# Kernel tuning notes

Measured on AMD Instinct MI355X. Metric: run time of the kernel, lower is better.

## Reference

```python
import jax, jax.numpy as jnp
import numpy as np


def setup_inputs() -> dict:
    key = jax.random.key(0)
    ks = jax.random.split(key, 6)
    B, Cx, Cf, Ch, H, W = 4, 512, 512, 256, 64, 64
    return {
        "query_features": jax.random.normal(ks[0], (B, Cx, H, W), dtype=jnp.float32),
        "reference_features": jax.random.normal(ks[1], (B, Cf, H, W), dtype=jnp.float32),
        "Wq": jax.random.normal(ks[2], (Ch, Cx), dtype=jnp.float32) * (1.0 / np.sqrt(Cx)),
        "bq": jax.random.normal(ks[3], (Ch,), dtype=jnp.float32) * 0.02,
        "Wk": jax.random.normal(ks[4], (Ch, Cf), dtype=jnp.float32) * (1.0 / np.sqrt(Cf)),
        "bk": jax.random.normal(ks[5], (Ch,), dtype=jnp.float32) * 0.02,
    }


def reference(query_features, reference_features, Wq, bq, Wk, bk):
    # 1x1 convs == per-pixel linear projections over channels
    Q = jnp.einsum('bchw,oc->bohw', query_features, Wq) + bq[None, :, None, None]
    K = jnp.einsum('bchw,oc->bohw', reference_features, Wk) + bk[None, :, None, None]
    B, Cf, H2, W2 = reference_features.shape
    H1, W1 = Q.shape[2], Q.shape[3]
    V = reference_features.reshape(B, Cf, H2 * W2)            # b c p
    # unscaled QK^T over hidden channels: [b, h1, w1, h2*w2]
    scores = jnp.einsum('bcij,bckl->bijkl', Q, K).reshape(B, H1, W1, H2 * W2)
    attn = jax.nn.softmax(scores, axis=-1)
    out = jnp.einsum('bijp,bcp->bcij', attn, V)               # [b, Cf, h1, w1]
    return out
```

## Files before the change

kernel.cpp:

```cpp
#include <hip/hip_runtime.h>
#include <hip/hip_bf16.h>
#include <hip/hip_fp16.h>

typedef _Float16 half8 __attribute__((ext_vector_type(8)));
typedef _Float16 half4v __attribute__((ext_vector_type(4)));
typedef float f4 __attribute__((ext_vector_type(4)));
typedef float f16v __attribute__((ext_vector_type(16)));
typedef short short8 __attribute__((ext_vector_type(8)));
typedef unsigned short us8 __attribute__((ext_vector_type(8)));
typedef int i4 __attribute__((ext_vector_type(4)));

#define P_SZ 4096
#define CH 256
#define CIN 512
#define CV 512
#define KVB 32
#define L2E 1.4426950408889634f

__device__ __forceinline__ unsigned short f2bf(float f) {
  unsigned u = __float_as_uint(f);
  unsigned r = u + 0x7fffu + ((u >> 16) & 1u);
  return (unsigned short)(r >> 16);
}
__device__ __forceinline__ float bf2f(unsigned short h) {
  return __uint_as_float(((unsigned)h) << 16);
}

__device__ __forceinline__ void gload16(const void* g, void* l) {
  __builtin_amdgcn_global_load_lds(
      (const __attribute__((address_space(1))) unsigned int*)g,
      (__attribute__((address_space(3))) unsigned int*)l, 16, 0, 0);
}

__global__ __launch_bounds__(256) void wconv_kernel(
    const float* __restrict__ Wq, const float* __restrict__ Wk,
    _Float16* __restrict__ Wf) {
  const int i = blockIdx.x * 256 + threadIdx.x;
  const int which = i >> 17;
  const int j = i & 131071;
  const float w = which ? Wk[j] : Wq[j] * L2E;
  Wf[i] = (_Float16)w;
}

__global__ __launch_bounds__(512) void proj_kernel(
    const float* __restrict__ Xq, const float* __restrict__ bq,
    const float* __restrict__ Xk, const float* __restrict__ bk,
    const _Float16* __restrict__ Wf,
    _Float16* __restrict__ Qout, _Float16* __restrict__ Kout,
    _Float16* __restrict__ Vout) {
  __shared__ float Xs[64][65];
  const int which = blockIdx.z;
  const float* __restrict__ X = which ? Xk : Xq;
  const float* __restrict__ bias = which ? bk : bq;
  _Float16* __restrict__ out = which ? Kout : Qout;
  const float bscale = which ? 1.f : L2E;

  const int b = blockIdx.y;
  const int p0 = blockIdx.x * 64;
  const int tid = threadIdx.x;
  const int w = tid >> 6, l = tid & 63;
  const int wp = w >> 2, wo = w & 3;
  const int lr = l & 15, lg = l >> 4;

  const float* __restrict__ Xb = X + (size_t)b * CIN * P_SZ;
  const _Float16* __restrict__ Wfb = Wf + (size_t)which * 131072;

  f4 acc[2][4];
  #pragma unroll
  for (int m = 0; m < 2; ++m)
    #pragma unroll
    for (int n = 0; n < 4; ++n) acc[m][n] = (f4){0.f, 0.f, 0.f, 0.f};

  const int crow = tid >> 4;
  const int pq4 = (tid & 15) * 4;

  #pragma unroll 1
  for (int kc64 = 0; kc64 < CIN; kc64 += 64) {
    __syncthreads();
    #pragma unroll
    for (int h2 = 0; h2 < 2; ++h2) {
      const int c = crow + h2 * 32;
      const f4 x = *(const f4*)(Xb + (size_t)(kc64 + c) * P_SZ + p0 + pq4);
      Xs[pq4 + 0][c] = x[0];
      Xs[pq4 + 1][c] = x[1];
      Xs[pq4 + 2][c] = x[2];
      Xs[pq4 + 3][c] = x[3];
    }
    __syncthreads();

    if (which == 1) {
      half8 v;
      #pragma unroll
      for (int j = 0; j < 8; ++j) v[j] = (_Float16)Xs[w * 8 + j][l];
      _Float16* vd = Vout + (size_t)b * 2097152 + (size_t)(p0 >> 5) * 16384
                   + (size_t)(w >> 2) * 16384 + (w & 3) * 4096 + (kc64 + l) * 8;
      *(half8*)vd = v;
    }

    #pragma unroll
    for (int s = 0; s < 2; ++s) {
      const int kc = kc64 + s * 32;
      half8 ah[2];
      #pragma unroll
      for (int m = 0; m < 2; ++m) {
        const int pl = wp * 32 + m * 16 + lr;
        #pragma unroll
        for (int i = 0; i < 8; ++i)
          ah[m][i] = (_Float16)Xs[pl][s * 32 + lg * 8 + i];
      }
      half8 bh[4];
      #pragma unroll
      for (int n = 0; n < 4; ++n) {
        const size_t wi = (size_t)(wo * 64 + n * 16 + lr) * CIN + kc + lg * 8;
        bh[n] = *(const half8*)(Wfb + wi);
      }
      #pragma unroll
      for (int m = 0; m < 2; ++m)
        #pragma unroll
        for (int n = 0; n < 4; ++n)
          acc[m][n] = __builtin_amdgcn_mfma_f32_16x16x32_f16(ah[m], bh[n], acc[m][n], 0, 0, 0);
    }
  }

  #pragma unroll
  for (int n = 0; n < 4; ++n) {
    const int o = wo * 64 + n * 16 + lr;
    const float bv = bias[o] * bscale;
    #pragma unroll
    for (int m = 0; m < 2; ++m) {
      #pragma unroll
      for (int j = 0; j < 4; ++j) {
        const int p = p0 + wp * 32 + m * 16 + lg * 4 + j;
        const _Float16 val = (_Float16)(acc[m][n][j] + bv);
        if (which == 0) {
          out[((size_t)b * P_SZ + p) * CH + o] = val;
        } else {
          const int kk = p & 31;
          const int kswz = (kk & 19) | ((kk & 4) << 1) | ((kk & 8) >> 1);
          out[(size_t)b * 1048576 + (size_t)(p >> 5) * 8192
              + (size_t)(o >> 3) * 256 + kswz * 8 + (o & 7)] = val;
        }
      }
    }
  }
}

template <int NSEG, bool DIRECT>
__global__ __launch_bounds__(512, 2) void attn_kernel(
    const _Float16* __restrict__ Qg, const _Float16* __restrict__ Kt,
    const _Float16* __restrict__ Vt, unsigned short* __restrict__ Opart,
    float* __restrict__ Mp, float* __restrict__ Lp, float* __restrict__ Og) {
  __shared__ char K_l[3][16384];
  __shared__ char V_l[3][32768];

  constexpr int nt = (P_SZ / NSEG) / KVB;
  int b, qt, seg;
  if (NSEG == 2) {
    const int g = blockIdx.x & 7;
    b = g >> 1; seg = g & 1; qt = blockIdx.x >> 3;
  } else {
    b = blockIdx.x & 3; seg = 0; qt = blockIdx.x >> 2;
  }

  const int tid = threadIdx.x;
  const int w = tid >> 6, l = tid & 63;
  const int hi = l >> 5, l31 = l & 31;
  const int wq = w >> 1, half = w & 1;

  const char* Kb = (const char*)Kt + (size_t)b * 2097152 + (size_t)seg * nt * 16384;
  const char* Vb = (const char*)Vt + (size_t)b * 4194304 + (size_t)seg * nt * 32768;

#define STAGE(BUF, T) do { \
    const char* ksrc = Kb + (size_t)(T) * 16384; \
    const char* vsrc = Vb + (size_t)(T) * 32768; \
    gload16(ksrc + tid * 16,         &K_l[BUF][w * 1024]); \
    gload16(ksrc + 8192 + tid * 16,  &K_l[BUF][8192 + w * 1024]); \
    gload16(vsrc + tid * 16,         &V_l[BUF][w * 1024]); \
    gload16(vsrc + 8192 + tid * 16,  &V_l[BUF][8192 + w * 1024]); \
    gload16(vsrc + 16384 + tid * 16, &V_l[BUF][16384 + w * 1024]); \
    gload16(vsrc + 24576 + tid * 16, &V_l[BUF][24576 + w * 1024]); \
  } while (0)

  half8 qf[16];
  {
    const char* qrow = (const char*)Qg +
        ((size_t)b * P_SZ + qt * 128 + wq * 32 + l31) * 512;
    #pragma unroll
    for (int m = 0; m < 16; ++m) qf[m] = *(const half8*)(qrow + m * 32 + hi * 16);
  }

  f16v acc[8];
  #pragma unroll
  for (int n = 0; n < 8; ++n)
    acc[n] = (f16v){0,0,0,0, 0,0,0,0, 0,0,0,0, 0,0,0,0};

  float m_run = -1e30f, lsum = 0.f;
  const int kread = hi * 512 + l31 * 16;
  const int vread = hi * 8192 + half * 4096 + l31 * 16;

  STAGE(0, 0); STAGE(1, 1);
  asm volatile("s_waitcnt vmcnt(6)" ::: "memory");
  asm volatile("s_barrier" ::: "memory");

  int bufc = 0;
  #pragma unroll 1
  for (int t = 0; t < nt; ++t) {
    const char* kb = &K_l[bufc][0] + kread;
    f16v s = (f16v){0,0,0,0, 0,0,0,0, 0,0,0,0, 0,0,0,0};
    __builtin_amdgcn_s_setprio(1);
    #pragma unroll
    for (int m = 0; m < 16; ++m) {
      half8 kf = *(const half8*)(kb + m * 1024);
      s = __builtin_amdgcn_mfma_f32_32x32x16_f16(kf, qf[m], s, 0, 0, 0);
    }
    __builtin_amdgcn_s_setprio(0);

    float x0 = fmaxf(s[0], s[8]),  x1 = fmaxf(s[1], s[9]);
    float x2 = fmaxf(s[2], s[10]), x3 = fmaxf(s[3], s[11]);
    float x4 = fmaxf(s[4], s[12]), x5 = fmaxf(s[5], s[13]);
    float x6 = fmaxf(s[6], s[14]), x7 = fmaxf(s[7], s[15]);
    x0 = fmaxf(x0, x4); x1 = fmaxf(x1, x5); x2 = fmaxf(x2, x6); x3 = fmaxf(x3, x7);
    float pm = fmaxf(fmaxf(x0, x1), fmaxf(x2, x3));
    pm = fmaxf(pm, __shfl_xor(pm, 32));
    if (__any(pm > m_run + 12.f)) {
      const float mnew = fmaxf(m_run, pm);
      const float al = __builtin_amdgcn_exp2f(m_run - mnew);
      const int alb = __float_as_int(al);
      #pragma unroll
      for (int r = 0; r < 16; ++r) {
        const int cr = (r & 3) + 8 * (r >> 2);
        const float ar = __int_as_float(
            __builtin_amdgcn_ds_bpermute(cr * 4 + hi * 16, alb));
        #pragma unroll
        for (int n = 0; n < 8; ++n) acc[n][r] *= ar;
      }
      lsum *= al;
      m_run = mnew;
    }
    float p[16], psum;
    #pragma unroll
    for (int r = 0; r < 16; ++r) p[r] = __builtin_amdgcn_exp2f(s[r] - m_run);
    {
      float a0 = (p[0] + p[1]) + (p[2] + p[3]);
      float a1 = (p[4] + p[5]) + (p[6] + p[7]);
      float a2 = (p[8] + p[9]) + (p[10] + p[11]);
      float a3 = (p[12] + p[13]) + (p[14] + p[15]);
      psum = (a0 + a1) + (a2 + a3);
      psum += __shfl_xor(psum, 32);
    }
    lsum += psum;

    i4 w0v, w1v;
    w0v[0] = __builtin_bit_cast(int, __builtin_amdgcn_cvt_pkrtz(p[0], p[1]));
    w0v[1] = __builtin_bit_cast(int, __builtin_amdgcn_cvt_pkrtz(p[2], p[3]));
    w0v[2] = __builtin_bit_cast(int, __builtin_amdgcn_cvt_pkrtz(p[4], p[5]));
    w0v[3] = __builtin_bit_cast(int, __builtin_amdgcn_cvt_pkrtz(p[6], p[7]));
    w1v[0] = __builtin_bit_cast(int, __builtin_amdgcn_cvt_pkrtz(p[8], p[9]));
    w1v[1] = __builtin_bit_cast(int, __builtin_amdgcn_cvt_pkrtz(p[10], p[11]));
    w1v[2] = __builtin_bit_cast(int, __builtin_amdgcn_cvt_pkrtz(p[12], p[13]));
    w1v[3] = __builtin_bit_cast(int, __builtin_amdgcn_cvt_pkrtz(p[14], p[15]));
    const half8 pa0 = __builtin_bit_cast(half8, w0v);
    const half8 pa1 = __builtin_bit_cast(half8, w1v);

    const int bufs = bufc == 0 ? 2 : bufc - 1;
    if (t + 2 < nt) STAGE(bufs, t + 2);

    const char* vb = &V_l[bufc][0] + vread;
    __builtin_amdgcn_s_setprio(1);
    #pragma unroll
    for (int n = 0; n < 8; ++n) {
      half8 v0 = *(const half8*)(vb + n * 512);
      acc[n] = __builtin_amdgcn_mfma_f32_32x32x16_f16(pa0, v0, acc[n], 0, 0, 0);
      half8 v1 = *(const half8*)(vb + 16384 + n * 512);
      acc[n] = __builtin_amdgcn_mfma_f32_32x32x16_f16(pa1, v1, acc[n], 0, 0, 0);
    }
    __builtin_amdgcn_s_setprio(0);

    if (t + 2 < nt) { asm volatile("s_waitcnt vmcnt(6)" ::: "memory"); }
    else            { asm volatile("s_waitcnt vmcnt(0)" ::: "memory"); }
    asm volatile("s_barrier" ::: "memory");
    bufc = bufc == 2 ? 0 : bufc + 1;
  }
#undef STAGE

  const int qg0 = qt * 128 + wq * 32;
  if (!DIRECT) {
    unsigned short* Ob = Opart +
        (((size_t)seg * 4 + b) * P_SZ + qg0) * 512 + half * 256 + l31;
    #pragma unroll
    for (int n = 0; n < 8; ++n) {
      #pragma unroll
      for (int r = 0; r < 16; ++r) {
        const int q = (r & 3) + 8 * (r >> 2) + 4 * hi;
        Ob[(size_t)q * 512 + n * 32] = f2bf(acc[n][r]);
      }
    }
    if (half == 0 && l < 32) {
      const size_t mi = ((size_t)seg * 4 + b) * P_SZ + qg0 + l31;
      Mp[mi] = m_run; Lp[mi] = lsum;
    }
  } else {
    float linv[16];
    const int lb = __float_as_int(lsum);
    #pragma unroll
    for (int r = 0; r < 16; ++r) {
      const int cr = (r & 3) + 8 * (r >> 2);
      const float lq = __int_as_float(__builtin_amdgcn_ds_bpermute(cr * 4 + hi * 16, lb));
      linv[r] = 1.f / lq;
    }
    #pragma unroll
    for (int n = 0; n < 8; ++n) {
      #pragma unroll
      for (int r = 0; r < 16; ++r) {
        const int q = (r & 3) + 8 * (r >> 2) + 4 * hi;
        Og[((size_t)b * CV + half * 256 + n * 32 + l31) * P_SZ + qg0 + q] =
            acc[n][r] * linv[r];
      }
    }
  }
}

template <int NSEG>
__global__ __launch_bounds__(256) void combine_kernel(
    const unsigned short* __restrict__ Opart, const float* __restrict__ Mp,
    const float* __restrict__ Lp, float* __restrict__ Og) {
  __shared__ float T[64][65];
  const int bx = blockIdx.x;
  const int ct = bx & 7, qt = (bx >> 3) & 63, b = bx >> 9;
  const int tid = threadIdx.x;
  {
    const int qi = tid >> 2, cj = tid & 3;
    const int q = qt * 64 + qi;
    const size_t mibase = (size_t)b * P_SZ + q;
    float M = -1e30f;
    #pragma unroll
    for (int s = 0; s < NSEG; ++s) M = fmaxf(M, Mp[(size_t)s * 4 * P_SZ + mibase]);
    float L = 0.f;
    float o[16];
    #pragma unroll
    for (int e = 0; e < 16; ++e) o[e] = 0.f;
    #pragma unroll
    for (int s = 0; s < NSEG; ++s) {
      const float wgt = __builtin_amdgcn_exp2f(Mp[(size_t)s * 4 * P_SZ + mibase] - M);
      L += wgt * Lp[(size_t)s * 4 * P_SZ + mibase];
      const unsigned short* src = Opart +
          (((size_t)s * 4 + b) * P_SZ + q) * 512 + ct * 64 + cj * 16;
      const us8 ua = ((const us8*)src)[0];
      const us8 ub = ((const us8*)src)[1];
      #pragma unroll
      for (int e = 0; e < 8; ++e) {
        o[e]     += wgt * bf2f(ua[e]);
        o[8 + e] += wgt * bf2f(ub[e]);
      }
    }
    const float inv = 1.f / L;
    #pragma unroll
    for (int e = 0; e < 16; ++e) T[qi][cj * 16 + e] = o[e] * inv;
  }
  __syncthreads();
  const int ci = tid >> 2, qj = tid & 3;
  #pragma unroll
  for (int i = 0; i < 4; ++i) {
    f4 v;
    #pragma unroll
    for (int e = 0; e < 4; ++e) v[e] = T[qj * 16 + i * 4 + e][ci];
    *(f4*)&Og[((size_t)b * CV + ct * 64 + ci) * P_SZ + qt * 64 + qj * 16 + i * 4] = v;
  }
}

extern "C" void kernel_launch(void* const* d_in, const int* in_sizes, int n_in,
                              void* d_out, int out_size, void* d_ws, size_t ws_size,
                              hipStream_t stream) {
  const float* x  = (const float*)d_in[0];
  const float* f  = (const float*)d_in[1];
  const float* Wq = (const float*)d_in[2];
  const float* bq = (const float*)d_in[3];
  const float* Wk = (const float*)d_in[4];
  const float* bk = (const float*)d_in[5];
  float* out = (float*)d_out;

  char* ws = (char*)d_ws;
  _Float16* Qf = (_Float16*)ws;
  _Float16* Kf = (_Float16*)(ws + ((size_t)8 << 20));
  _Float16* Vf = (_Float16*)(ws + ((size_t)16 << 20));
  float* Mp    = (float*)(ws + ((size_t)32 << 20));
  float* Lp    = (float*)(ws + ((size_t)32 << 20) + (256 << 10));
  _Float16* Wf = (_Float16*)(ws + ((size_t)32 << 20) + (512 << 10));
  unsigned short* Opart = (unsigned short*)(ws + ((size_t)34 << 20));

  wconv_kernel<<<dim3(1024), dim3(256), 0, stream>>>(Wq, Wk, Wf);
  proj_kernel<<<dim3(64, 4, 2), dim3(512), 0, stream>>>(x, bq, f, bk, Wf, Qf, Kf, Vf);

  const size_t need2 = ((size_t)34 << 20) + ((size_t)32 << 20);
  const size_t need1 = ((size_t)34 << 20) + ((size_t)16 << 20);
  if (ws_size >= need2) {
    attn_kernel<2, false><<<dim3(256), dim3(512), 0, stream>>>(Qf, Kf, Vf, Opart, Mp, Lp, nullptr);
    combine_kernel<2><<<dim3(2048), dim3(256), 0, stream>>>(Opart, Mp, Lp, out);
  } else if (ws_size >= need1) {
    attn_kernel<1, false><<<dim3(128), dim3(512), 0, stream>>>(Qf, Kf, Vf, Opart, Mp, Lp, nullptr);
    combine_kernel<1><<<dim3(2048), dim3(256), 0, stream>>>(Opart, Mp, Lp, out);
  } else {
    attn_kernel<1, true><<<dim3(128), dim3(512), 0, stream>>>(Qf, Kf, Vf, nullptr, nullptr, nullptr, out);
  }
}
```

Baseline: 210.7 us.

## Fuse split-KV combine into attention kernel via last-block atomic counter

Removes the separate combine kernel for the two-segment path. Each attention block writes its partial output, then bumps an atomic counter per (batch, query tile). The block that arrives second merges both partials using the running max and sum, transposes the result through shared memory, and writes the final fp32 output. This saves one kernel launch and lets the combine overlap with other blocks' attention work, at the cost of a memset launch, fences, and serialized combine work in the last blocks.

```diff
diff --git a/kernel.cpp b/kernel.cpp
--- a/kernel.cpp
+++ b/kernel.cpp
@@ -145,13 +145,15 @@
   }
 }
 
-template <int NSEG, bool DIRECT>
+template <int NSEG, int MODE>
 __global__ __launch_bounds__(512, 2) void attn_kernel(
     const _Float16* __restrict__ Qg, const _Float16* __restrict__ Kt,
     const _Float16* __restrict__ Vt, unsigned short* __restrict__ Opart,
-    float* __restrict__ Mp, float* __restrict__ Lp, float* __restrict__ Og) {
+    float* __restrict__ Mp, float* __restrict__ Lp, float* __restrict__ Og,
+    int* __restrict__ flags) {
   __shared__ char K_l[3][16384];
   __shared__ char V_l[3][32768];
+  __shared__ int is_last_sh;
 
   constexpr int nt = (P_SZ / NSEG) / KVB;
   int b, qt, seg;
@@ -284,7 +286,7 @@
 #undef STAGE
 
   const int qg0 = qt * 128 + wq * 32;
-  if (!DIRECT) {
+  if (MODE != 1) {
     unsigned short* Ob = Opart +
         (((size_t)seg * 4 + b) * P_SZ + qg0) * 512 + half * 256 + l31;
     #pragma unroll
@@ -298,6 +300,63 @@
     if (half == 0 && l < 32) {
       const size_t mi = ((size_t)seg * 4 + b) * P_SZ + qg0 + l31;
       Mp[mi] = m_run; Lp[mi] = lsum;
+    }
+    if (MODE == 2) {
+      __threadfence();
+      if (tid == 0) is_last_sh = atomicAdd(&flags[b * 32 + qt], 1);
+      __syncthreads();
+      if (is_last_sh == 1) {
+        __threadfence();
+        float* Tb = (float*)(&K_l[0][0]) + (tid >> 8) * (64 * 65);
+        const int t2 = tid & 255;
+        #pragma unroll 1
+        for (int rnd = 0; rnd < 8; ++rnd) {
+          const int t16 = rnd * 2 + (tid >> 8);
+          const int qh = t16 >> 3, ct = t16 & 7;
+          const int q64 = qt * 128 + qh * 64;
+          {
+            const int qi = t2 >> 2, cj = t2 & 3;
+            const int q = q64 + qi;
+            const size_t i0 = (size_t)b * P_SZ + q;
+            const size_t i1 = (size_t)(4 + b) * P_SZ + q;
+            const float M = fmaxf(Mp[i0], Mp[i1]);
+            float L = 0.f;
+            float o[16];
+            #pragma unroll
+            for (int e = 0; e < 16; ++e) o[e] = 0.f;
+            #pragma unroll
+            for (int sdx = 0; sdx < 2; ++sdx) {
+              const size_t mi = sdx ? i1 : i0;
+              const float wgt = __builtin_amdgcn_exp2f(Mp[mi] - M);
+              L += wgt * Lp[mi];
+              const unsigned short* src = Opart +
+                  (((size_t)sdx * 4 + b) * P_SZ + q) * 512 + ct * 64 + cj * 16;
+              const us8 ua = ((const us8*)src)[0];
+              const us8 ub = ((const us8*)src)[1];
+              #pragma unroll
+              for (int e = 0; e < 8; ++e) {
+                o[e]     += wgt * bf2f(ua[e]);
+                o[8 + e] += wgt * bf2f(ub[e]);
+              }
+            }
+            const float inv = 1.f / L;
+            #pragma unroll
+            for (int e = 0; e < 16; ++e) Tb[qi * 65 + cj * 16 + e] = o[e] * inv;
+          }
+          __syncthreads();
+          {
+            const int ci = t2 >> 2, qj = t2 & 3;
+            #pragma unroll
+            for (int i = 0; i < 4; ++i) {
+              f4 v;
+              #pragma unroll
+              for (int e = 0; e < 4; ++e) v[e] = Tb[(qj * 16 + i * 4 + e) * 65 + ci];
+              *(f4*)&Og[((size_t)b * CV + ct * 64 + ci) * P_SZ + q64 + qj * 16 + i * 4] = v;
+            }
+          }
+          __syncthreads();
+        }
+      }
     }
   } else {
     float linv[16];
@@ -386,6 +445,7 @@
   float* Mp    = (float*)(ws + ((size_t)32 << 20));
   float* Lp    = (float*)(ws + ((size_t)32 << 20) + (256 << 10));
   _Float16* Wf = (_Float16*)(ws + ((size_t)32 << 20) + (512 << 10));
+  int* flags   = (int*)(ws + ((size_t)33 << 20));
   unsigned short* Opart = (unsigned short*)(ws + ((size_t)34 << 20));
 
   wconv_kernel<<<dim3(1024), dim3(256), 0, stream>>>(Wq, Wk, Wf);
@@ -394,12 +454,12 @@
   const size_t need2 = ((size_t)34 << 20) + ((size_t)32 << 20);
   const size_t need1 = ((size_t)34 << 20) + ((size_t)16 << 20);
   if (ws_size >= need2) {
-    attn_kernel<2, false><<<dim3(256), dim3(512), 0, stream>>>(Qf, Kf, Vf, Opart, Mp, Lp, nullptr);
-    combine_kernel<2><<<dim3(2048), dim3(256), 0, stream>>>(Opart, Mp, Lp, out);
+    hipMemsetAsync(flags, 0, 128 * sizeof(int), stream);
+    attn_kernel<2, 2><<<dim3(256), dim3(512), 0, stream>>>(Qf, Kf, Vf, Opart, Mp, Lp, out, flags);
   } else if (ws_size >= need1) {
-    attn_kernel<1, false><<<dim3(128), dim3(512), 0, stream>>>(Qf, Kf, Vf, Opart, Mp, Lp, nullptr);
+    attn_kernel<1, 0><<<dim3(128), dim3(512), 0, stream>>>(Qf, Kf, Vf, Opart, Mp, Lp, nullptr, nullptr);
     combine_kernel<1><<<dim3(2048), dim3(256), 0, stream>>>(Opart, Mp, Lp, out);
   } else {
-    attn_kernel<1, true><<<dim3(128), dim3(512), 0, stream>>>(Qf, Kf, Vf, nullptr, nullptr, nullptr, out);
-  }
-}
+    attn_kernel<1, 1><<<dim3(128), dim3(512), 0, stream>>>(Qf, Kf, Vf, nullptr, nullptr, nullptr, out, nullptr);
+  }
+}
```

Result: slower. 315.2 us (+49.6%).
